# Kernel tuning notes

Measured on AMD Instinct MI355X. Metric: run time of the kernel, lower is better.

Reference implementation:

```python
import jax, jax.numpy as jnp
import numpy as np

D = 4096       # hidden_size
H = 32         # n_heads (tp_size=1)
DN = 128       # qk_nope_head_dim
DR = 64        # qk_rope_head_dim
DV = 128       # v_head_dim
QL = 1536      # q_lora_rank
KL = 512       # kv_lora_rank
S = 2048       # seqlen, start_pos = 0
EPS = 1e-6
SCALE = (DN + DR) ** -0.5  # softmax_scale (no yarn mscale: seqlen <= original_seq_len)
THETA = 10000.0


def _freqs(seqlen, dim, base=THETA):
    # precompute_freqs_cis without yarn correction (seqlen <= original_seq_len)
    inv = 1.0 / (base ** (np.arange(0, dim, 2, dtype=np.float32) / dim))
    f = np.outer(np.arange(seqlen, dtype=np.float32), inv)  # [S, dim//2]
    return jnp.asarray(np.cos(f)), jnp.asarray(np.sin(f))


def _rmsnorm(x, w):
    return x * jax.lax.rsqrt(jnp.mean(x * x, axis=-1, keepdims=True) + EPS) * w


def _rope(x, cos, sin):
    # x: [S, H, R]; complex rotation on consecutive pairs (view_as_complex semantics)
    S_, H_, R_ = x.shape
    xr = x.reshape(S_, H_, R_ // 2, 2)
    x0, x1 = xr[..., 0], xr[..., 1]
    c = cos[:, None, :]
    s = sin[:, None, :]
    y0 = x0 * c - x1 * s
    y1 = x0 * s + x1 * c
    return jnp.stack([y0, y1], axis=-1).reshape(S_, H_, R_)


def setup_inputs() -> dict:
    key = jax.random.key(0)
    ks = jax.random.split(key, 6)
    std = 0.02
    return {
        "x": jax.random.normal(ks[0], (S, D), jnp.float32),
        "wq_a": jax.random.normal(ks[1], (QL, D), jnp.float32) * std,
        "q_norm_w": jnp.ones((QL,), jnp.float32),
        "wq_b": jax.random.normal(ks[2], (H * (DN + DR), QL), jnp.float32) * std,
        "wkv_a": jax.random.normal(ks[3], (KL + DR, D), jnp.float32) * std,
        "kv_norm_w": jnp.ones((KL,), jnp.float32),
        "wkv_b": jax.random.normal(ks[4], (H * (DN + DV), KL), jnp.float32) * std,
        "wo": jax.random.normal(ks[5], (D, H * DV), jnp.float32) * std,
    }


def reference(x, wq_a, q_norm_w, wq_b, wkv_a, kv_norm_w, wkv_b, wo):
    cos, sin = _freqs(S, DR)

    # q path: low-rank down-proj + RMSNorm + up-proj
    q = _rmsnorm(x @ wq_a.T, q_norm_w) @ wq_b.T          # [S, H*(DN+DR)]
    q = q.reshape(S, H, DN + DR)
    q_nope, q_pe = q[..., :DN], q[..., DN:]
    q_pe = _rope(q_pe, cos, sin)                          # [S, H, DR]

    # kv path: joint latent + rope part
    kv_all = x @ wkv_a.T                                  # [S, KL+DR]
    kv = _rmsnorm(kv_all[:, :KL], kv_norm_w)              # latent kv cache [S, KL]
    k_pe = _rope(kv_all[:, None, KL:], cos, sin)[:, 0, :]  # pe cache [S, DR]

    # absorb k-up-projection into q (einsum 'shd,hdc->shc')
    wkv_b_r = wkv_b.reshape(H, DN + DV, KL)
    q_lat = jnp.einsum("shd,hdc->shc", q_nope, wkv_b_r[:, :DN])  # [S, H, KL]

    scores = (jnp.einsum("shc,tc->sht", q_lat, kv)
              + jnp.einsum("shr,tr->sht", q_pe, k_pe)) * SCALE   # [S, H, T]

    causal = jnp.arange(S)[:, None] >= jnp.arange(S)[None, :]     # [S, T]
    scores = jnp.where(causal[:, None, :], scores, -jnp.inf)
    p = jax.nn.softmax(scores, axis=-1)

    o_lat = jnp.einsum("sht,tc->shc", p, kv)                      # [S, H, KL]
    o = jnp.einsum("shc,hdc->shd", o_lat, wkv_b_r[:, DN:])        # [S, H, DV]
    return o.reshape(S, H * DV) @ wo.T                            # [S, D]
```

## Files before the change

kernel.cpp:

```cpp
#include <hip/hip_runtime.h>
#include <hip/hip_bf16.h>
#include <type_traits>

using bf16 = __hip_bfloat16;
typedef short v8s __attribute__((ext_vector_type(8)));
typedef float v4f __attribute__((ext_vector_type(4)));

#define DEV __device__ __forceinline__

constexpr float SCALE_ = 0.07216878364870322f;

DEV unsigned short bfu(float f) {
  bf16 h = __float2bfloat16(f);
  return __builtin_bit_cast(unsigned short, h);
}
DEV float b2f(short u) {
  unsigned int x = ((unsigned int)(unsigned short)u) << 16;
  return __builtin_bit_cast(float, x);
}

DEV void g2lds16(const void* g, void* l) {
  __builtin_amdgcn_global_load_lds(
      (const __attribute__((address_space(1))) unsigned int*)g,
      (__attribute__((address_space(3))) unsigned int*)l, 16, 0, 0);
}


__global__ void cast_kernel(const float* __restrict__ in, bf16* __restrict__ out, int n4) {
  int i = blockIdx.x * 256 + threadIdx.x;
  int stride = gridDim.x * 256;
  for (; i < n4; i += stride) {
    float4 v = ((const float4*)in)[i];
    ushort4 u;
    u.x = bfu(v.x); u.y = bfu(v.y); u.z = bfu(v.z); u.w = bfu(v.w);
    ((ushort4*)out)[i] = u;
  }
}

__global__ void cast_pad_kernel(const float* __restrict__ in, bf16* __restrict__ out) {
  int i = blockIdx.x * 256 + threadIdx.x;
  float4 v = make_float4(0.f, 0.f, 0.f, 0.f);
  if (i < 589824) v = ((const float4*)in)[i];
  ushort4 u;
  u.x = bfu(v.x); u.y = bfu(v.y); u.z = bfu(v.z); u.w = bfu(v.w);
  ((ushort4*)out)[i] = u;
}

__global__ void wkvbt_kernel(const float* __restrict__ wkvb, bf16* __restrict__ out) {
  int i = blockIdx.x * 256 + threadIdx.x;
  int d = i & 127, c = (i >> 7) & 511, h = i >> 16;
  out[i] = __float2bfloat16(wkvb[(h * 256 + d) * 512 + c]);
}

__global__ void wkvbv_kernel(const float* __restrict__ wkvb, bf16* __restrict__ out) {
  int i = blockIdx.x * 256 + threadIdx.x;
  int c4 = i & 127, d = (i >> 7) & 127, h = i >> 14;
  float4 v = *(const float4*)(wkvb + ((long)(h * 256 + 128 + d)) * 512 + c4 * 4);
  ushort4 u;
  u.x = bfu(v.x); u.y = bfu(v.y); u.z = bfu(v.z); u.w = bfu(v.w);
  *(ushort4*)(out + ((long)(h * 128 + d)) * 512 + c4 * 4) = u;
}

__global__ void freqs_kernel(float* __restrict__ cosb, float* __restrict__ sinb) {
  int t = blockIdx.x * 256 + threadIdx.x;
  int s = t >> 5, i = t & 31;
  float inv = powf(10000.0f, -(float)(2 * i) / 64.0f);
  float f = (float)s * inv;
  cosb[t] = cosf(f);
  sinb[t] = sinf(f);
}

__global__ void rmsnorm_bf_kernel(const bf16* __restrict__ in, const float* __restrict__ w,
                                  bf16* __restrict__ out, int L, int ldin, int ldout) {
  int row = blockIdx.x;
  const bf16* x = in + (long)row * ldin;
  int L8 = L >> 3;
  float ss = 0.f;
  for (int i = threadIdx.x; i < L8; i += 256) {
    v8s v = *(const v8s*)(x + i * 8);
#pragma unroll
    for (int j = 0; j < 8; ++j) { float f = b2f(v[j]); ss += f * f; }
  }
#pragma unroll
  for (int d = 1; d < 64; d <<= 1) ss += __shfl_xor(ss, d);
  __shared__ float red[4];
  if ((threadIdx.x & 63) == 0) red[threadIdx.x >> 6] = ss;
  __syncthreads();
  float r = rsqrtf((red[0] + red[1] + red[2] + red[3]) / (float)L + 1e-6f);
  bf16* o = out + (long)row * ldout;
  for (int i = threadIdx.x; i < L8; i += 256) {
    v8s v = *(const v8s*)(x + i * 8);
    v8s u;
#pragma unroll
    for (int j = 0; j < 8; ++j)
      u[j] = (short)bfu(b2f(v[j]) * r * w[i * 8 + j]);
    *(v8s*)(o + i * 8) = u;
  }
}

__global__ void rope_kpe_kernel(const bf16* __restrict__ kvall, const float* __restrict__ cosb,
                                const float* __restrict__ sinb, bf16* __restrict__ keff) {
  int t = blockIdx.x * 256 + threadIdx.x;
  int s = t >> 5, i = t & 31;
  const bf16* p = kvall + (long)s * 640 + 512;
  float x0 = __bfloat162float(p[2 * i]), x1 = __bfloat162float(p[2 * i + 1]);
  float c = cosb[t], sn = sinb[t];
  bf16* o = keff + (long)s * 576 + 512;
  o[2 * i] = __float2bfloat16(x0 * c - x1 * sn);
  o[2 * i + 1] = __float2bfloat16(x0 * sn + x1 * c);
}

__global__ void qnope_cast_kernel(const bf16* __restrict__ qf, bf16* __restrict__ qnope) {
  int i = blockIdx.x * 256 + threadIdx.x;
  int d8 = i & 15, h = (i >> 4) & 31, s = i >> 9;
  *(v8s*)(qnope + (long)s * 4096 + h * 128 + d8 * 8) =
      *(const v8s*)(qf + (long)s * 6144 + h * 192 + d8 * 8);
}

__global__ void rope_q_kernel(const bf16* __restrict__ qf, const float* __restrict__ cosb,
                              const float* __restrict__ sinb, bf16* __restrict__ qeff) {
  int t = blockIdx.x * 256 + threadIdx.x;
  int i = t & 31, h = (t >> 5) & 31, s = t >> 10;
  const bf16* p = qf + (long)s * 6144 + h * 192 + 128;
  float x0 = __bfloat162float(p[2 * i]), x1 = __bfloat162float(p[2 * i + 1]);
  float c = cosb[s * 32 + i], sn = sinb[s * 32 + i];
  bf16* o = qeff + (long)s * 18432 + h * 576 + 512;
  o[2 * i] = __float2bfloat16(x0 * c - x1 * sn);
  o[2 * i + 1] = __float2bfloat16(x0 * sn + x1 * c);
}

__global__ void vtrans_kernel(const bf16* __restrict__ keff, bf16* __restrict__ vT) {
  int gid = blockIdx.x * 256 + threadIdx.x;
  int t8 = (gid & 255) * 8, c8 = (gid >> 8) * 8;
  v8s in[8];
#pragma unroll
  for (int r = 0; r < 8; ++r)
    in[r] = *(const v8s*)(keff + (long)(t8 + r) * 576 + c8);
#pragma unroll
  for (int cc = 0; cc < 8; ++cc) {
    v8s o;
#pragma unroll
    for (int r = 0; r < 8; ++r) o[r] = in[r][cc];
    *(v8s*)(vT + (long)(c8 + cc) * 2048 + t8) = o;
  }
}

template <typename OutT>
__global__ __launch_bounds__(256, 3) void gemm_bt(
    const bf16* __restrict__ A, const bf16* __restrict__ B, OutT* __restrict__ C,
    int K, int lda, int ldb, int ldc, long sA, long sB, long sC) {
  __shared__ bf16 lA[4096];
  __shared__ bf16 lB[4096];
  const int tid = threadIdx.x;
  const int lane = tid & 63;
  const int w = tid >> 6, wm = w >> 1, wn = w & 1;
  const int r16 = lane & 15, kg = (lane >> 4) << 3;
  const int arow = tid >> 2, acol = (tid & 3) << 3;
  const bf16* Ab = A + (long)blockIdx.z * sA + (long)blockIdx.y * 128 * lda;
  const bf16* Bb = B + (long)blockIdx.z * sB + (long)blockIdx.x * 128 * ldb;
  v4f acc[4][4] = {};
  for (int k0 = 0; k0 < K; k0 += 32) {
    __syncthreads();
#pragma unroll
    for (int i = 0; i < 2; ++i) {
      g2lds16(Ab + (long)(i * 64 + arow) * lda + (k0 + acol), &lA[i * 2048 + w * 512]);
      g2lds16(Bb + (long)(i * 64 + arow) * ldb + (k0 + acol), &lB[i * 2048 + w * 512]);
    }
    __syncthreads();
    v8s af[4], bfr[4];
#pragma unroll
    for (int mi = 0; mi < 4; ++mi)
      af[mi] = *(const v8s*)&lA[(wm * 64 + mi * 16 + r16) * 32 + kg];
#pragma unroll
    for (int ni = 0; ni < 4; ++ni)
      bfr[ni] = *(const v8s*)&lB[(wn * 64 + ni * 16 + r16) * 32 + kg];
    __builtin_amdgcn_s_setprio(1);
#pragma unroll
    for (int mi = 0; mi < 4; ++mi)
#pragma unroll
      for (int ni = 0; ni < 4; ++ni)
        acc[mi][ni] = __builtin_amdgcn_mfma_f32_16x16x32_bf16(af[mi], bfr[ni], acc[mi][ni], 0, 0, 0);
    __builtin_amdgcn_s_setprio(0);
  }
  OutT* Cb = C + (long)blockIdx.z * sC + (long)(blockIdx.y * 128) * ldc + blockIdx.x * 128;
  const int cr = (lane >> 4) << 2;
#pragma unroll
  for (int mi = 0; mi < 4; ++mi)
#pragma unroll
    for (int ni = 0; ni < 4; ++ni)
#pragma unroll
      for (int j = 0; j < 4; ++j) {
        long idx = (long)(wm * 64 + mi * 16 + cr + j) * ldc + wn * 64 + ni * 16 + r16;
        float v = acc[mi][ni][j];
        if constexpr (std::is_same<OutT, float>::value) Cb[idx] = v;
        else Cb[idx] = __float2bfloat16(v);
      }
}

__global__ __launch_bounds__(512, 2) void attn_kernel(
    const bf16* __restrict__ qeff, const bf16* __restrict__ keff,
    const bf16* __restrict__ vT, bf16* __restrict__ olat) {
  __shared__ __align__(16) bf16 kl[32 * 576];
  __shared__ __align__(16) bf16 vl[512 * 32];
  const int tid = threadIdx.x, lane = tid & 63, w = tid >> 6;
  const int r16 = lane & 15, hi = lane >> 4;
  const int kg = hi << 3, cr = hi << 2;
  const int lb = blockIdx.y * 16 + blockIdx.x;
  const int p = lb & 255;
  const int g = p >> 5;
  const int h = p & 31;
  const int qt = (lb < 256) ? (15 - g) : g;
  const int qrow = qt * 128 + w * 16 + r16;
  const int rb = r16 & 7;

  const long qbase = (long)qrow * 18432 + h * 576;
  v8s qreg[18];
#pragma unroll
  for (int kk = 0; kk < 18; ++kk)
    qreg[kk] = __builtin_nontemporal_load((const v8s*)(qeff + qbase + kk * 32 + kg));

  v4f acc[32] = {};
  float mrow = -1e30f, lrow = 0.f;

  auto stageK = [&](int t0) {
#pragma unroll
    for (int it = 0; it < 5; ++it) {
      int D = it * 512 + tid;
      if (D < 2304) {
        int row = D / 72;
        int gg = D - row * 72;
        int gs = gg ^ (row & 7);
        g2lds16(keff + (long)(t0 + row) * 576 + gs * 8,
                (char*)kl + (it * 512 + w * 64) * 16);
      }
    }
  };
  auto stageV = [&](int t0) {
#pragma unroll
    for (int it = 0; it < 4; ++it) {
      int D = it * 512 + tid;
      int row = D >> 2;
      int s = (D & 3) ^ ((row >> 1) & 3);
      g2lds16(vT + (long)row * 2048 + t0 + s * 8,
              (char*)vl + (it * 512 + w * 64) * 16);
    }
  };

  const int nch = 4 * qt + 4;
  stageK(0);
  __syncthreads();

  for (int kc = 0; kc < nch; ++kc) {
    const int t0 = kc * 32;
    stageV(t0);

    const char* kb = (const char*)kl;
    v4f sf0 = {}, sf1 = {};
    __builtin_amdgcn_s_setprio(1);
#pragma unroll
    for (int kk = 0; kk < 18; ++kk) {
      int so = ((kk * 4 + hi) ^ rb) << 4;
      v8s b0 = *(const v8s*)(kb + r16 * 1152 + so);
      v8s b1 = *(const v8s*)(kb + (16 + r16) * 1152 + so);
      sf0 = __builtin_amdgcn_mfma_f32_16x16x32_bf16(b0, qreg[kk], sf0, 0, 0, 0);
      sf1 = __builtin_amdgcn_mfma_f32_16x16x32_bf16(b1, qreg[kk], sf1, 0, 0, 0);
    }
    __builtin_amdgcn_s_setprio(0);
    float s0[4], s1[4];
#pragma unroll
    for (int j = 0; j < 4; ++j) { s0[j] = sf0[j] * SCALE_; s1[j] = sf1[j] * SCALE_; }
    if (kc >= 4 * qt) {
#pragma unroll
      for (int j = 0; j < 4; ++j) {
        if (t0 + cr + j > qrow) s0[j] = -1e30f;
        if (t0 + 16 + cr + j > qrow) s1[j] = -1e30f;
      }
    }
    float mx = fmaxf(fmaxf(fmaxf(s0[0], s0[1]), fmaxf(s0[2], s0[3])),
                     fmaxf(fmaxf(s1[0], s1[1]), fmaxf(s1[2], s1[3])));
    mx = fmaxf(mx, __shfl_xor(mx, 16));
    mx = fmaxf(mx, __shfl_xor(mx, 32));
    if (!__all(mx <= mrow + 8.0f)) {
      float mn = fmaxf(mrow, mx);
      float alpha = __expf(mrow - mn);
      mrow = mn;
      lrow *= alpha;
      float af0 = __shfl(alpha, cr + 0), af1 = __shfl(alpha, cr + 1);
      float af2 = __shfl(alpha, cr + 2), af3 = __shfl(alpha, cr + 3);
#pragma unroll
      for (int c = 0; c < 32; ++c) {
        acc[c][0] *= af0; acc[c][1] *= af1; acc[c][2] *= af2; acc[c][3] *= af3;
      }
    }
    float p0[4], p1[4];
#pragma unroll
    for (int j = 0; j < 4; ++j) {
      p0[j] = __expf(s0[j] - mrow);
      p1[j] = __expf(s1[j] - mrow);
    }
    float rs = (p0[0] + p0[1]) + (p0[2] + p0[3]) + (p1[0] + p1[1]) + (p1[2] + p1[3]);
    rs += __shfl_xor(rs, 16);
    rs += __shfl_xor(rs, 32);
    lrow += rs;
    int u0 = (int)((unsigned)bfu(p0[0]) | ((unsigned)bfu(p0[1]) << 16));
    int u1 = (int)((unsigned)bfu(p0[2]) | ((unsigned)bfu(p0[3]) << 16));
    int v0 = (int)((unsigned)bfu(p1[0]) | ((unsigned)bfu(p1[1]) << 16));
    int v1 = (int)((unsigned)bfu(p1[2]) | ((unsigned)bfu(p1[3]) << 16));
    const int L1 = r16 + 32 * (hi & 1);
    const int L2 = L1 + 16;
    const bool lo = hi < 2;
    int d0a = __shfl(u0, L1), d0b = __shfl(v0, L1);
    int d1a = __shfl(u1, L1), d1b = __shfl(v1, L1);
    int d2a = __shfl(u0, L2), d2b = __shfl(v0, L2);
    int d3a = __shfl(u1, L2), d3b = __shfl(v1, L2);
    int4 pw = make_int4(lo ? d0a : d0b, lo ? d1a : d1b, lo ? d2a : d2b, lo ? d3a : d3b);
    v8s ap = __builtin_bit_cast(v8s, pw);

    __syncthreads();
    if (kc + 1 < nch) stageK(t0 + 32);

    __builtin_amdgcn_s_setprio(1);
#pragma unroll
    for (int c = 0; c < 32; ++c) {
      const int vrow = c * 16 + r16;
      const int vsw = (hi ^ ((vrow >> 1) & 3)) << 4;
      v8s bv = *(const v8s*)((const char*)vl + vrow * 64 + vsw);
      acc[c] = __builtin_amdgcn_mfma_f32_16x16x32_bf16(ap, bv, acc[c], 0, 0, 0);
    }
    __builtin_amdgcn_s_setprio(0);
    __syncthreads();
  }
  float linv0 = 1.0f / __shfl(lrow, cr + 0);
  float linv1 = 1.0f / __shfl(lrow, cr + 1);
  float linv2 = 1.0f / __shfl(lrow, cr + 2);
  float linv3 = 1.0f / __shfl(lrow, cr + 3);
  unsigned short* ou = (unsigned short*)olat;
  const long ob = (long)(qt * 128 + w * 16 + cr) * 16384 + h * 512 + r16;
#pragma unroll
  for (int c = 0; c < 32; ++c) {
    __builtin_nontemporal_store(bfu(acc[c][0] * linv0), ou + ob + 0 * 16384 + c * 16);
    __builtin_nontemporal_store(bfu(acc[c][1] * linv1), ou + ob + 1 * 16384 + c * 16);
    __builtin_nontemporal_store(bfu(acc[c][2] * linv2), ou + ob + 2 * 16384 + c * 16);
    __builtin_nontemporal_store(bfu(acc[c][3] * linv3), ou + ob + 3 * 16384 + c * 16);
  }
}


extern "C" void kernel_launch(void* const* d_in, const int* in_sizes, int n_in,
                              void* d_out, int out_size, void* d_ws, size_t ws_size,
                              hipStream_t stream) {
  const float* x = (const float*)d_in[0];
  const float* wq_a = (const float*)d_in[1];
  const float* q_norm_w = (const float*)d_in[2];
  const float* wq_b = (const float*)d_in[3];
  const float* wkv_a = (const float*)d_in[4];
  const float* kv_norm_w = (const float*)d_in[5];
  const float* wkv_b = (const float*)d_in[6];
  const float* wo = (const float*)d_in[7];
  char* ws = (char*)d_ws;

  float* cosb  = (float*)(ws + 0);
  float* sinb  = (float*)(ws + 262144);
  bf16* qeffb  = (bf16*)(ws + 524288);
  bf16* olat   = (bf16*)(ws + 76021760);
  bf16* keff   = (bf16*)(ws + 143130624);
  bf16* vTb    = (bf16*)(ws + 145489920);
  bf16* xb     = (bf16*)(ws + 76021760);
  bf16* wqab   = (bf16*)(ws + 92798976);
  bf16* wkvabp = (bf16*)(ws + 105381888);
  bf16* qa     = (bf16*)(ws + 110624768);
  bf16* kvall  = (bf16*)(ws + 116916224);
  bf16* qan    = (bf16*)(ws + 125829120);
  bf16* wqbb   = (bf16*)(ws + 76021760);
  bf16* qf     = (bf16*)(ws + 94896128);
  bf16* qnope  = (bf16*)(ws + 120061952);
  bf16* wkvb1t = (bf16*)(ws + 76021760);
  bf16* wkvbv  = (bf16*)(ws + 524288);
  bf16* obuf   = (bf16*)(ws + 4718592);
  bf16* wob    = (bf16*)(ws + 21495808);

  cast_kernel<<<2048, 256, 0, stream>>>(x, xb, 2097152);
  cast_kernel<<<2048, 256, 0, stream>>>(wq_a, wqab, 1572864);
  cast_pad_kernel<<<2560, 256, 0, stream>>>(wkv_a, wkvabp);
  freqs_kernel<<<256, 256, 0, stream>>>(cosb, sinb);

  gemm_bt<bf16><<<dim3(12, 16, 1), 256, 0, stream>>>(xb, wqab, qa, 4096, 4096, 4096, 1536, 0, 0, 0);
  gemm_bt<bf16><<<dim3(5, 16, 1), 256, 0, stream>>>(xb, wkvabp, kvall, 4096, 4096, 4096, 640, 0, 0, 0);

  rmsnorm_bf_kernel<<<2048, 256, 0, stream>>>(qa, q_norm_w, qan, 1536, 1536, 1536);
  rmsnorm_bf_kernel<<<2048, 256, 0, stream>>>(kvall, kv_norm_w, keff, 512, 640, 576);
  rope_kpe_kernel<<<256, 256, 0, stream>>>(kvall, cosb, sinb, keff);
  vtrans_kernel<<<64, 256, 0, stream>>>(keff, vTb);

  cast_kernel<<<2048, 256, 0, stream>>>(wq_b, wqbb, 2359296);
  gemm_bt<bf16><<<dim3(48, 16, 1), 256, 0, stream>>>(qan, wqbb, qf, 1536, 1536, 1536, 6144, 0, 0, 0);

  qnope_cast_kernel<<<4096, 256, 0, stream>>>(qf, qnope);
  rope_q_kernel<<<8192, 256, 0, stream>>>(qf, cosb, sinb, qeffb);
  wkvbt_kernel<<<8192, 256, 0, stream>>>(wkv_b, wkvb1t);
  gemm_bt<bf16><<<dim3(4, 16, 32), 256, 0, stream>>>(qnope, wkvb1t, qeffb,
      128, 4096, 128, 18432, 128L, 65536L, 576L);

  attn_kernel<<<dim3(16, 32), 512, 0, stream>>>(qeffb, keff, vTb, olat);

  wkvbv_kernel<<<2048, 256, 0, stream>>>(wkv_b, wkvbv);
  gemm_bt<bf16><<<dim3(1, 16, 32), 256, 0, stream>>>(olat, wkvbv, obuf,
      512, 16384, 512, 4096, 512L, 65536L, 128L);

  cast_kernel<<<2048, 256, 0, stream>>>(wo, wob, 4194304);
  gemm_bt<float><<<dim3(32, 16, 1), 256, 0, stream>>>(obuf, wob, (float*)d_out,
      4096, 4096, 4096, 4096, 0, 0, 0);
}
```

Baseline: 744.4 us.

## Drop qnope copy kernel, tile wkv_b transpose, use plain stores for o_lat

The q_nope copy kernel is removed. The absorption GEMM now reads q_nope directly from the q projection output using a row stride of 6144 and a per-head offset of 192. The wkv_b transpose kernel is rewritten so each thread loads an 8x8 tile with float4 reads and writes 8 contiguous bf16 values, replacing scattered scalar reads. The attention epilogue switches from nontemporal stores to ordinary bf16 stores, so o_lat may stay in cache for the following GEMM. Together these cut one launch and one intermediate buffer, at the cost of a less compact A operand for the GEMM.

```diff
diff --git a/kernel.cpp b/kernel.cpp
--- a/kernel.cpp
+++ b/kernel.cpp
@@ -47,9 +47,27 @@
 }
 
 __global__ void wkvbt_kernel(const float* __restrict__ wkvb, bf16* __restrict__ out) {
-  int i = blockIdx.x * 256 + threadIdx.x;
-  int d = i & 127, c = (i >> 7) & 511, h = i >> 16;
-  out[i] = __float2bfloat16(wkvb[(h * 256 + d) * 512 + c]);
+  int gid = blockIdx.x * 256 + threadIdx.x;
+  int c8 = (gid & 63) * 8;
+  int d8 = ((gid >> 6) & 15) * 8;
+  int h = gid >> 10;
+  float4 a[8][2];
+#pragma unroll
+  for (int r = 0; r < 8; ++r) {
+    const float* p = wkvb + ((long)(h * 256 + d8 + r)) * 512 + c8;
+    a[r][0] = *(const float4*)p;
+    a[r][1] = *(const float4*)(p + 4);
+  }
+#pragma unroll
+  for (int cc = 0; cc < 8; ++cc) {
+    v8s o;
+#pragma unroll
+    for (int r = 0; r < 8; ++r) {
+      float f = (cc < 4) ? ((const float*)&a[r][0])[cc] : ((const float*)&a[r][1])[cc - 4];
+      o[r] = (short)bfu(f);
+    }
+    *(v8s*)(out + (long)h * 65536 + (c8 + cc) * 128 + d8) = o;
+  }
 }
 
 __global__ void wkvbv_kernel(const float* __restrict__ wkvb, bf16* __restrict__ out) {
@@ -108,13 +126,6 @@
   bf16* o = keff + (long)s * 576 + 512;
   o[2 * i] = __float2bfloat16(x0 * c - x1 * sn);
   o[2 * i + 1] = __float2bfloat16(x0 * sn + x1 * c);
-}
-
-__global__ void qnope_cast_kernel(const bf16* __restrict__ qf, bf16* __restrict__ qnope) {
-  int i = blockIdx.x * 256 + threadIdx.x;
-  int d8 = i & 15, h = (i >> 4) & 31, s = i >> 9;
-  *(v8s*)(qnope + (long)s * 4096 + h * 128 + d8 * 8) =
-      *(const v8s*)(qf + (long)s * 6144 + h * 192 + d8 * 8);
 }
 
 __global__ void rope_q_kernel(const bf16* __restrict__ qf, const float* __restrict__ cosb,
@@ -334,14 +345,13 @@
   float linv1 = 1.0f / __shfl(lrow, cr + 1);
   float linv2 = 1.0f / __shfl(lrow, cr + 2);
   float linv3 = 1.0f / __shfl(lrow, cr + 3);
-  unsigned short* ou = (unsigned short*)olat;
   const long ob = (long)(qt * 128 + w * 16 + cr) * 16384 + h * 512 + r16;
 #pragma unroll
   for (int c = 0; c < 32; ++c) {
-    __builtin_nontemporal_store(bfu(acc[c][0] * linv0), ou + ob + 0 * 16384 + c * 16);
-    __builtin_nontemporal_store(bfu(acc[c][1] * linv1), ou + ob + 1 * 16384 + c * 16);
-    __builtin_nontemporal_store(bfu(acc[c][2] * linv2), ou + ob + 2 * 16384 + c * 16);
-    __builtin_nontemporal_store(bfu(acc[c][3] * linv3), ou + ob + 3 * 16384 + c * 16);
+    olat[ob + 0 * 16384 + c * 16] = __float2bfloat16(acc[c][0] * linv0);
+    olat[ob + 1 * 16384 + c * 16] = __float2bfloat16(acc[c][1] * linv1);
+    olat[ob + 2 * 16384 + c * 16] = __float2bfloat16(acc[c][2] * linv2);
+    olat[ob + 3 * 16384 + c * 16] = __float2bfloat16(acc[c][3] * linv3);
   }
 }
 
@@ -373,7 +383,6 @@
   bf16* qan    = (bf16*)(ws + 125829120);
   bf16* wqbb   = (bf16*)(ws + 76021760);
   bf16* qf     = (bf16*)(ws + 94896128);
-  bf16* qnope  = (bf16*)(ws + 120061952);
   bf16* wkvb1t = (bf16*)(ws + 76021760);
   bf16* wkvbv  = (bf16*)(ws + 524288);
   bf16* obuf   = (bf16*)(ws + 4718592);
@@ -395,11 +404,10 @@
   cast_kernel<<<2048, 256, 0, stream>>>(wq_b, wqbb, 2359296);
   gemm_bt<bf16><<<dim3(48, 16, 1), 256, 0, stream>>>(qan, wqbb, qf, 1536, 1536, 1536, 6144, 0, 0, 0);
 
-  qnope_cast_kernel<<<4096, 256, 0, stream>>>(qf, qnope);
   rope_q_kernel<<<8192, 256, 0, stream>>>(qf, cosb, sinb, qeffb);
-  wkvbt_kernel<<<8192, 256, 0, stream>>>(wkv_b, wkvb1t);
-  gemm_bt<bf16><<<dim3(4, 16, 32), 256, 0, stream>>>(qnope, wkvb1t, qeffb,
-      128, 4096, 128, 18432, 128L, 65536L, 576L);
+  wkvbt_kernel<<<128, 256, 0, stream>>>(wkv_b, wkvb1t);
+  gemm_bt<bf16><<<dim3(4, 16, 32), 256, 0, stream>>>(qf, wkvb1t, qeffb,
+      128, 6144, 128, 18432, 192L, 65536L, 576L);
 
   attn_kernel<<<dim3(16, 32), 512, 0, stream>>>(qeffb, keff, vTb, olat);
 
```

Measured after the change: 727.9 us. 2.2% less time.
